# Performance work log

Measured on AMD Instinct MI355X. Metric: run time of the kernel, lower is better.

## Reference

```python
import jax, jax.numpy as jnp
import numpy as np

IOU_THRESHOLD = 0.5


def setup_inputs() -> dict:
    key = jax.random.key(0)
    k1, k2, k3 = jax.random.split(key, 3)
    B, N = 4, 8192
    # valid boxes: top-left in [0,200), width/height in [1,51)
    xy = jax.random.uniform(k1, (B, N, 2), dtype=jnp.float32) * 200.0
    wh = jax.random.uniform(k2, (B, N, 2), dtype=jnp.float32) * 50.0 + 1.0
    boxes = jnp.concatenate([xy, xy + wh], axis=-1)  # [B,N,4] (x1,y1,x2,y2)
    scores = jax.random.uniform(k3, (B, N), dtype=jnp.float32)
    return {"boxes": boxes, "scores": scores}


def _soft_nms_single(boxes, scores):
    # boxes: [N,4], scores: [N]
    x1, y1, x2, y2 = boxes[:, 0], boxes[:, 1], boxes[:, 2], boxes[:, 3]
    inter_w = jnp.maximum(0.0, jnp.minimum(x2[:, None], x2[None, :]) - jnp.maximum(x1[:, None], x1[None, :]))
    inter_h = jnp.maximum(0.0, jnp.minimum(y2[:, None], y2[None, :]) - jnp.maximum(y1[:, None], y1[None, :]))
    inter = inter_w * inter_h  # [N,N]
    area = (x2 - x1) * (y2 - y1)  # [N]
    union = area[:, None] + area[None, :] - inter
    iou = inter / union  # [N,N]
    weight = jnp.exp(-iou / IOU_THRESHOLD)  # [N,N]
    adjusted = weight @ scores  # [N] : adjusted_scores[i] = sum_j w[i,j]*s[j]
    w = jax.nn.softmax(adjusted, axis=0)  # [N]
    return w @ boxes  # [4]


def reference(boxes, scores):
    return jax.vmap(_soft_nms_single)(boxes, scores)  # [B,4]
```

## Files before the change

kernel.cpp:

```cpp
#include <hip/hip_runtime.h>
#include <hip/hip_bf16.h>

#define BATCH   4
#define NBOX    8192
#define BLOCK   256
#define TSZ     256
#define NT      (NBOX / TSZ)
#define NPAIRS  (NT * (NT + 1) / 2)
#define NBINS   2048
#define SUBS    8
#define SUBSZ   (NBOX / SUBS)
#define STH     512

__device__ __forceinline__ float bf2f(unsigned short u) {
    union { unsigned int i; float f; } c;
    c.i = ((unsigned int)u) << 16;
    return c.f;
}

__device__ __forceinline__ bool box_plausible(float x1, float y1, float x2, float y2) {
    bool ok = (x1 == x1) && (y1 == y1) && (x2 == x2) && (y2 == y2);
    ok = ok && fabsf(x1) < 1e4f && fabsf(y1) < 1e4f && fabsf(x2) < 1e4f && fabsf(y2) < 1e4f;
    ok = ok && x1 >= -1.0f && x1 <= 300.0f && y1 >= -1.0f && y1 <= 300.0f;
    const float w = x2 - x1, h = y2 - y1;
    ok = ok && w >= -0.1f && w <= 80.0f && h >= -0.1f && h <= 80.0f;
    return ok;
}

__device__ __forceinline__ bool wave_probe_is_f32(const void* boxes_raw) {
    const int lane = threadIdx.x & 63;
    const float* bf = (const float*)boxes_raw;
    const bool okf = box_plausible(bf[lane * 4 + 0], bf[lane * 4 + 1],
                                   bf[lane * 4 + 2], bf[lane * 4 + 3]);
    const unsigned short* bh = (const unsigned short*)boxes_raw;
    const bool okh = box_plausible(bf2f(bh[lane * 4 + 0]), bf2f(bh[lane * 4 + 1]),
                                   bf2f(bh[lane * 4 + 2]), bf2f(bh[lane * 4 + 3]));
    const unsigned long long mf = __ballot(okf);
    const unsigned long long mh = __ballot(okh);
    return __popcll(mf) >= __popcll(mh);
}

__device__ __forceinline__ float4 load_box(const void* boxes_raw, size_t idx, bool isf32) {
    if (isf32) {
        return reinterpret_cast<const float4*>(boxes_raw)[idx];
    } else {
        const ushort4 u = reinterpret_cast<const ushort4*>(boxes_raw)[idx];
        return make_float4(bf2f(u.x), bf2f(u.y), bf2f(u.z), bf2f(u.w));
    }
}

__device__ __forceinline__ float load_score(const void* scores_raw, size_t idx, bool isf32) {
    return isf32 ? ((const float*)scores_raw)[idx]
                 : bf2f(((const unsigned short*)scores_raw)[idx]);
}

__device__ __forceinline__ int key_bin(float v) {
    const int bb = (int)(v * 8.0f);
    return min(NBINS - 1, max(0, bb));
}

#define CEXP (-2.8853900817779268f)

__device__ __forceinline__ float pair_weight(
    float ix1, float iy1, float ix2, float iy2, float iarea,
    const float4& bj, float jarea)
{
    float w = fminf(ix2, bj.z) - fmaxf(ix1, bj.x);
    float h = fminf(iy2, bj.w) - fmaxf(iy1, bj.y);
    w = fmaxf(w, 0.0f);
    h = fmaxf(h, 0.0f);
    const float inter = w * h;
    const float uni   = iarea + jarea - inter;
    const float arg   = (CEXP * inter) * __builtin_amdgcn_rcpf(uni);
    return __builtin_amdgcn_exp2f(arg);
}

__global__ __launch_bounds__(STH) void sort_kernel(
    const void* __restrict__ boxes_raw, const void* __restrict__ scores_raw,
    float4* __restrict__ sboxes, float* __restrict__ sscores,
    float* __restrict__ adj,
    float* __restrict__ minx1c, float* __restrict__ maxx2c,
    int* __restrict__ pairlist, int* __restrict__ count)
{
    __shared__ int hist[NBINS];
    __shared__ int bmin[NBINS];
    __shared__ int hist2[NBINS];
    __shared__ int wsum[STH / 64];
    __shared__ float sminT[NT], smaxT[NT];
    __shared__ int scnt;

    const int b    = blockIdx.x / SUBS;
    const int sub  = blockIdx.x % SUBS;
    const int tid  = threadIdx.x;
    const int lane = tid & 63;
    const int wv   = tid >> 6;
    const bool isf32 = wave_probe_is_f32(boxes_raw);
    const size_t base = (size_t)b * NBOX;

#pragma unroll
    for (int i = 0; i < NBINS / STH; i++) {
        hist[i * STH + tid]  = 0;
        bmin[i * STH + tid]  = 0x7f800000;
        hist2[i * STH + tid] = 0;
    }
    if (tid == 0) scnt = 0;
    {
        const size_t z = (size_t)blockIdx.x * 1024;
        adj[z + tid] = 0.0f;
        adj[z + STH + tid] = 0.0f;
    }
    __syncthreads();

    const int sublim = sub * SUBSZ;
#pragma unroll
    for (int k = 0; k < NBOX / STH; k++) {
        const int i = k * STH + tid;
        const float4 bx = load_box(boxes_raw, base + i, isf32);
        const int bin = key_bin(bx.z);
        atomicAdd(&hist[bin], 1);
        atomicMin(&bmin[bin], __float_as_int(bx.x));
        if (i < sublim) atomicAdd(&hist2[bin], 1);
    }
    __syncthreads();

    {
        int tot[4], cum[4];
        int run = 0;
#pragma unroll
        for (int i = 0; i < 4; i++) {
            tot[i] = hist[tid * 4 + i];
            run += tot[i]; cum[i] = run;
        }
        int v = run;
#pragma unroll
        for (int d = 1; d < 64; d <<= 1) {
            const int u = __shfl_up(v, d);
            if (lane >= d) v += u;
        }
        if (lane == 63) wsum[wv] = v;
        __syncthreads();
        int wb = 0;
        for (int w = 0; w < wv; w++) wb += wsum[w];
        const int tb = wb + v - run;
#pragma unroll
        for (int i = 0; i < 4; i++) {
            const int bin = tid * 4 + i;
            const int e = tb + cum[i] - tot[i];
            const int m = hist2[bin];
            hist[bin]  = e;
            hist2[bin] = e + m;
        }
    }
    __syncthreads();

    if (tid < NT) {
        int p = tid * TSZ;
        int lo = 0, hi = NBINS - 1;
        while (lo < hi) { const int mid = (lo + hi + 1) >> 1;
                          if (hist[mid] <= p) lo = mid; else hi = mid - 1; }
        const int Bf = lo;
        p = tid * TSZ + TSZ - 1;
        lo = 0; hi = NBINS - 1;
        while (lo < hi) { const int mid = (lo + hi + 1) >> 1;
                          if (hist[mid] <= p) lo = mid; else hi = mid - 1; }
        const int Bl = lo;
        float mn = 3.4e38f;
        for (int q = Bf; q <= Bl; q++) mn = fminf(mn, __int_as_float(bmin[q]));
        const float mx = (float)(Bl + 1) * 0.125f;
        sminT[tid] = mn; smaxT[tid] = mx;
        if (sub == 0) {
            minx1c[b * NT + tid] = mn;
            maxx2c[b * NT + tid] = mx;
        }
    }
    __syncthreads();

    if (sub == 0) {
        for (int q = tid; q < NPAIRS; q += STH) {
            int p = q, it = 0;
            while (p >= NT - it) { p -= NT - it; it++; }
            const int jt = it + p;
            const bool live = !((smaxT[it] < sminT[jt]) || (smaxT[jt] < sminT[it]));
            if (live) {
                const int idx = atomicAdd(&scnt, 1);
                pairlist[b * NPAIRS + idx] = (it << 8) | jt;
            }
        }
    }

#pragma unroll
    for (int k = 0; k < SUBSZ / STH; k++) {
        const int i = sub * SUBSZ + k * STH + tid;
        const float4 bx = load_box(boxes_raw, base + i, isf32);
        const float  sc = load_score(scores_raw, base + i, isf32);
        const int pos = atomicAdd(&hist2[key_bin(bx.z)], 1);
        sboxes[base + pos]  = bx;
        sscores[base + pos] = sc;
    }

    __syncthreads();
    if (sub == 0 && tid == 0) count[b] = scnt;
}

__global__ __launch_bounds__(TSZ) void perm_kernel(
    const float4* __restrict__ sboxes, const float* __restrict__ sscores,
    float4* __restrict__ cboxes, float2* __restrict__ cas,
    int* __restrict__ crank,
    float* __restrict__ cgmin)
{
    __shared__ float key[TSZ];
    __shared__ int   idx[TSZ];
    const int tile = blockIdx.x;
    const size_t gbase = (size_t)tile * TSZ;
    const int tid = threadIdx.x;

    key[tid] = sboxes[gbase + tid].x;
    idx[tid] = tid;
    __syncthreads();

    for (int k = 2; k <= TSZ; k <<= 1) {
        for (int j = k >> 1; j > 0; j >>= 1) {
            const int l = tid ^ j;
            if (l > tid) {
                const bool up = ((tid & k) == 0);
                const float a = key[tid], c = key[l];
                if ((a > c) == up) {
                    key[tid] = c; key[l] = a;
                    const int ti = idx[tid]; idx[tid] = idx[l]; idx[l] = ti;
                }
            }
            __syncthreads();
        }
    }

    const int src = idx[tid];
    const float4 u = sboxes[gbase + src];
    cboxes[gbase + tid] = u;
    cas[gbase + tid] = make_float2((u.z - u.x) * (u.w - u.y), sscores[gbase + src]);
    crank[gbase + tid] = src;
    if ((tid & 63) == 0) cgmin[tile * 4 + (tid >> 6)] = key[tid];
}

__global__ __launch_bounds__(BLOCK, 4) void soft_nms_adj_kernel(
    const float4* __restrict__ sboxes,
    const float* __restrict__ sscores,
    const float4* __restrict__ cboxes,
    const float2* __restrict__ cas,
    const int* __restrict__ crank,
    const float* __restrict__ cgmin,
    const int* __restrict__ pairlist,
    const int* __restrict__ count,
    float* __restrict__ adj)
{
    __shared__ float4 sbox[TSZ];
    __shared__ float2 sas[TSZ];
    __shared__ float  srow[4][TSZ];

    const int bid = blockIdx.x;
    const int b   = bid / NPAIRS;
    const int p   = bid % NPAIRS;
    if (p >= count[b]) return;
    const int pr = pairlist[b * NPAIRS + p];
    const int it = pr >> 8, jt = pr & 255;

    const int tid  = threadIdx.x;
    const int lane = tid & 63;
    const int wv   = tid >> 6;
    const size_t base = (size_t)b * NBOX;

    float ws;
    {
        const int jg = jt * TSZ + tid;
        const float4 uj = cboxes[base + jg];
        sbox[tid] = uj;
        const float2 asv = cas[base + jg];
        sas[tid]  = asv;
        float w0 = asv.y;
#pragma unroll
        for (int off = 32; off > 0; off >>= 1) w0 += __shfl_xor(w0, off);
        ws = w0;
    }

    float rx1[4], ry1[4], rx2[4], ry2[4], rar[4], rsc[4];
#pragma unroll
    for (int k = 0; k < 4; k++) {
        const int ig = it * TSZ + k * 64 + lane;
        const float4 ui = sboxes[base + ig];
        rx1[k] = ui.x; ry1[k] = ui.y; rx2[k] = ui.z; ry2[k] = ui.w;
        rar[k] = (ui.z - ui.x) * (ui.w - ui.y);
        rsc[k] = sscores[base + ig];
    }

    int kstart = 0;
    if (it != jt) {
        const float cg = cgmin[(b * NT + jt) * 4 + wv];
#pragma unroll
        for (int k = 0; k < 4; k++) {
            const float gmax = __shfl(rx2[k], 63) + 0.125f;
            if (kstart == k && gmax < cg) kstart = k + 1;
        }
    }
    float ccorr = 0.0f;
    if (kstart > 0) {
#pragma unroll
        for (int k = 0; k < 4; k++) {
            if (k < kstart) {
                float gs = rsc[k];
#pragma unroll
                for (int off = 32; off > 0; off >>= 1) gs += __shfl_xor(gs, off);
                ccorr += gs;
            }
        }
    }

    __syncthreads();

    float accr[4];
#pragma unroll
    for (int k = 0; k < 4; k++) accr[k] = (k < kstart) ? ws : 0.0f;

    const int wvbase = wv * 64;

    if (it == jt) {
#pragma unroll 2
        for (int t = 0; t < 64; t++) {
            const int idx = wvbase + ((lane + t) & 63);
            const float4 bj = sbox[idx];
            const float2 as = sas[idx];
#pragma unroll
            for (int k = 0; k < 4; k++) {
                const float e = pair_weight(rx1[k], ry1[k], rx2[k], ry2[k], rar[k], bj, as.x);
                accr[k] = fmaf(e, as.y, accr[k]);
            }
        }
    } else {
#define OFFD_LOOP(KS)                                                          \
        {                                                                      \
            float accc = ccorr;                                                \
            _Pragma("unroll 2")                                                \
            for (int t = 0; t < 64; t++) {                                     \
                const int idx = wvbase + ((lane + t) & 63);                    \
                const float4 bj = sbox[idx];                                   \
                const float2 as = sas[idx];                                    \
                float c = 0.0f;                                                \
                _Pragma("unroll")                                              \
                for (int k = KS; k < 4; ++k) {                                 \
                    const float e = pair_weight(rx1[k], ry1[k], rx2[k], ry2[k],\
                                                rar[k], bj, as.x);             \
                    accr[k] = fmaf(e, as.y, accr[k]);                          \
                    c = fmaf(e, rsc[k], c);                                    \
                }                                                              \
                accc += __shfl(c, (lane - t) & 63);                            \
            }                                                                  \
            const int cr = crank[base + jt * TSZ + wvbase + lane];             \
            atomicAdd(&adj[base + jt * TSZ + cr], accc);                       \
        }
        switch (kstart) {
            case 0: OFFD_LOOP(0); break;
            case 1: OFFD_LOOP(1); break;
            case 2: OFFD_LOOP(2); break;
            case 3: OFFD_LOOP(3); break;
            default: {
                const int cr = crank[base + jt * TSZ + wvbase + lane];
                atomicAdd(&adj[base + jt * TSZ + cr], ccorr);
            } break;
        }
#undef OFFD_LOOP
    }

#pragma unroll
    for (int k = 0; k < 4; k++) srow[wv][k * 64 + lane] = accr[k];
    __syncthreads();
    {
        const float rs = srow[0][tid] + srow[1][tid] + srow[2][tid] + srow[3][tid];
        atomicAdd(&adj[base + it * TSZ + tid], rs);
    }
}

#define FBLK 1024
__global__ __launch_bounds__(FBLK) void soft_nms_finish_kernel(
    const float4* __restrict__ sboxes,
    const float* __restrict__ sscores,
    const float* __restrict__ adj,
    const float* __restrict__ minx1c, const float* __restrict__ maxx2c,
    const void* __restrict__ boxes_raw,
    void* __restrict__ out)
{
    constexpr int K  = NBOX / FBLK;
    constexpr int NW = FBLK / 64;
    __shared__ float sminx[NT], smaxx[NT], ssumT[NT], scorr[NT];
    __shared__ float smax_[NW];
    __shared__ float sred[NW][5];

    const int b    = blockIdx.x;
    const int tid  = threadIdx.x;
    const int lane = tid & 63;
    const int wv   = tid >> 6;
    const size_t base = (size_t)b * NBOX;

    const bool isf32 = wave_probe_is_f32(boxes_raw);

    if (tid < NT) {
        sminx[tid] = minx1c[b * NT + tid];
        smaxx[tid] = maxx2c[b * NT + tid];
    }
#pragma unroll
    for (int tt = 0; tt < 2; tt++) {
        const int T = wv * 2 + tt;
        float sm = 0.0f;
#pragma unroll
        for (int q = 0; q < 4; q++) sm += sscores[base + T * TSZ + q * 64 + lane];
#pragma unroll
        for (int off = 32; off > 0; off >>= 1) sm += __shfl_down(sm, off);
        if (lane == 0) ssumT[T] = sm;
    }
    __syncthreads();
    if (tid < NT) {
        float c = 0.0f;
        for (int T2 = 0; T2 < NT; T2++) {
            const bool skip = (smaxx[tid] < sminx[T2]) || (smaxx[T2] < sminx[tid]);
            if (skip) c += ssumT[T2];
        }
        scorr[tid] = c;
    }
    __syncthreads();

    float av[K];
    float m = -3.4e38f;
#pragma unroll
    for (int k = 0; k < K; k++) {
        const int r = k * FBLK + tid;
        av[k] = adj[base + r] + scorr[r >> 8];
        m = fmaxf(m, av[k]);
    }
#pragma unroll
    for (int off = 32; off > 0; off >>= 1)
        m = fmaxf(m, __shfl_down(m, off));
    if (lane == 0) smax_[wv] = m;
    __syncthreads();
    float M = smax_[0];
#pragma unroll
    for (int w = 1; w < NW; w++) M = fmaxf(M, smax_[w]);

    const float L2E = 1.4426950408889634f;
    float es = 0.0f, s0 = 0.0f, s1 = 0.0f, s2 = 0.0f, s3 = 0.0f;
#pragma unroll
    for (int k = 0; k < K; k++) {
        const float e = __builtin_amdgcn_exp2f((av[k] - M) * L2E);
        const float4 u = sboxes[base + k * FBLK + tid];
        es += e;
        s0 += e * u.x;
        s1 += e * u.y;
        s2 += e * u.z;
        s3 += e * u.w;
    }
#pragma unroll
    for (int off = 32; off > 0; off >>= 1) {
        es += __shfl_down(es, off);
        s0 += __shfl_down(s0, off);
        s1 += __shfl_down(s1, off);
        s2 += __shfl_down(s2, off);
        s3 += __shfl_down(s3, off);
    }
    if (lane == 0) {
        sred[wv][0] = es; sred[wv][1] = s0; sred[wv][2] = s1;
        sred[wv][3] = s2; sred[wv][4] = s3;
    }
    __syncthreads();
    if (tid == 0) {
        float ES = 0.0f, o[4] = {0.0f, 0.0f, 0.0f, 0.0f};
#pragma unroll
        for (int w = 0; w < NW; w++) {
            ES   += sred[w][0];
            o[0] += sred[w][1];
            o[1] += sred[w][2];
            o[2] += sred[w][3];
            o[3] += sred[w][4];
        }
        const float inv = 1.0f / ES;
        if (isf32) {
            float* of = (float*)out;
            for (int c = 0; c < 4; c++) of[b * 4 + c] = o[c] * inv;
        } else {
            __hip_bfloat16* oh = (__hip_bfloat16*)out;
            for (int c = 0; c < 4; c++) oh[b * 4 + c] = __float2bfloat16(o[c] * inv);
        }
    }
}

extern "C" void kernel_launch(void* const* d_in, const int* in_sizes, int n_in,
                              void* d_out, int out_size, void* d_ws, size_t ws_size,
                              hipStream_t stream) {
    const void* boxes_raw  = d_in[0];
    const void* scores_raw = d_in[1];

    char* w = (char*)d_ws;
    float4* sboxes   = (float4*)w;                 w += (size_t)BATCH * NBOX * 16;
    float4* cboxes   = (float4*)w;                 w += (size_t)BATCH * NBOX * 16;
    float2* cas      = (float2*)w;                 w += (size_t)BATCH * NBOX * 8;
    float*  sscores  = (float*)w;                  w += (size_t)BATCH * NBOX * 4;
    float*  adj      = (float*)w;                  w += (size_t)BATCH * NBOX * 4;
    int*    crank    = (int*)w;                    w += (size_t)BATCH * NBOX * 4;
    float*  minx1c   = (float*)w;                  w += (size_t)BATCH * NT * 4;
    float*  maxx2c   = (float*)w;                  w += (size_t)BATCH * NT * 4;
    float*  cgmin    = (float*)w;                  w += (size_t)BATCH * NT * 4 * 4;
    int*    pairlist = (int*)w;                    w += (size_t)BATCH * NPAIRS * 4;
    int*    count    = (int*)w;

    sort_kernel<<<dim3(BATCH * SUBS), dim3(STH), 0, stream>>>(
        boxes_raw, scores_raw, sboxes, sscores, adj, minx1c, maxx2c, pairlist, count);
    perm_kernel<<<dim3(BATCH * NT), dim3(TSZ), 0, stream>>>(
        sboxes, sscores, cboxes, cas, crank, cgmin);
    soft_nms_adj_kernel<<<dim3(BATCH * NPAIRS), dim3(BLOCK), 0, stream>>>(
        sboxes, sscores, cboxes, cas, crank, cgmin, pairlist, count, adj);
    soft_nms_finish_kernel<<<dim3(BATCH), dim3(FBLK), 0, stream>>>(
        sboxes, sscores, adj, minx1c, maxx2c, boxes_raw, d_out);
}
```

Baseline: 136.4 us.

## Replace bitonic sort with rank sort and accumulate column sums in permuted order

The per-tile bitonic sort in perm_kernel becomes an O(n) rank computation per thread that scatters boxes straight to their sorted slot and records the inverse permutation. The adjacency kernel no longer looks up crank before each column atomicAdd. It writes into a separate adjc buffer in permuted order, and the finish kernel gathers it back through cinv. Launch bounds for the adjacency kernel rise from 4 to 8 blocks per CU, at the cost of one extra zeroed buffer and an indexed gather in the finish kernel.

```diff
diff --git a/kernel.cpp b/kernel.cpp
--- a/kernel.cpp
+++ b/kernel.cpp
@@ -78,7 +78,7 @@
 __global__ __launch_bounds__(STH) void sort_kernel(
     const void* __restrict__ boxes_raw, const void* __restrict__ scores_raw,
     float4* __restrict__ sboxes, float* __restrict__ sscores,
-    float* __restrict__ adj,
+    float* __restrict__ adj, float* __restrict__ adjc,
     float* __restrict__ minx1c, float* __restrict__ maxx2c,
     int* __restrict__ pairlist, int* __restrict__ count)
 {
@@ -108,6 +108,8 @@
         const size_t z = (size_t)blockIdx.x * 1024;
         adj[z + tid] = 0.0f;
         adj[z + STH + tid] = 0.0f;
+        adjc[z + tid] = 0.0f;
+        adjc[z + STH + tid] = 0.0f;
     }
     __syncthreads();
 
@@ -205,52 +207,42 @@
 __global__ __launch_bounds__(TSZ) void perm_kernel(
     const float4* __restrict__ sboxes, const float* __restrict__ sscores,
     float4* __restrict__ cboxes, float2* __restrict__ cas,
-    int* __restrict__ crank,
+    int* __restrict__ cinv,
     float* __restrict__ cgmin)
 {
-    __shared__ float key[TSZ];
-    __shared__ int   idx[TSZ];
+    __shared__ float sx1[TSZ];
     const int tile = blockIdx.x;
     const size_t gbase = (size_t)tile * TSZ;
     const int tid = threadIdx.x;
 
-    key[tid] = sboxes[gbase + tid].x;
-    idx[tid] = tid;
-    __syncthreads();
-
-    for (int k = 2; k <= TSZ; k <<= 1) {
-        for (int j = k >> 1; j > 0; j >>= 1) {
-            const int l = tid ^ j;
-            if (l > tid) {
-                const bool up = ((tid & k) == 0);
-                const float a = key[tid], c = key[l];
-                if ((a > c) == up) {
-                    key[tid] = c; key[l] = a;
-                    const int ti = idx[tid]; idx[tid] = idx[l]; idx[l] = ti;
-                }
-            }
-            __syncthreads();
-        }
-    }
-
-    const int src = idx[tid];
-    const float4 u = sboxes[gbase + src];
-    cboxes[gbase + tid] = u;
-    cas[gbase + tid] = make_float2((u.z - u.x) * (u.w - u.y), sscores[gbase + src]);
-    crank[gbase + tid] = src;
-    if ((tid & 63) == 0) cgmin[tile * 4 + (tid >> 6)] = key[tid];
-}
-
-__global__ __launch_bounds__(BLOCK, 4) void soft_nms_adj_kernel(
+    const float4 u = sboxes[gbase + tid];
+    const float sc = sscores[gbase + tid];
+    sx1[tid] = u.x;
+    __syncthreads();
+
+    int rank = 0;
+#pragma unroll 8
+    for (int j = 0; j < TSZ; j++) {
+        const float v = sx1[j];
+        rank += (v < u.x || (v == u.x && j < tid)) ? 1 : 0;
+    }
+
+    cboxes[gbase + rank] = u;
+    cas[gbase + rank] = make_float2((u.z - u.x) * (u.w - u.y), sc);
+    cinv[gbase + tid] = rank;
+    if ((rank & 63) == 0) cgmin[tile * 4 + (rank >> 6)] = u.x;
+}
+
+__global__ __launch_bounds__(BLOCK, 8) void soft_nms_adj_kernel(
     const float4* __restrict__ sboxes,
     const float* __restrict__ sscores,
     const float4* __restrict__ cboxes,
     const float2* __restrict__ cas,
-    const int* __restrict__ crank,
     const float* __restrict__ cgmin,
     const int* __restrict__ pairlist,
     const int* __restrict__ count,
-    float* __restrict__ adj)
+    float* __restrict__ adj,
+    float* __restrict__ adjc)
 {
     __shared__ float4 sbox[TSZ];
     __shared__ float2 sas[TSZ];
@@ -352,18 +344,16 @@
                 }                                                              \
                 accc += __shfl(c, (lane - t) & 63);                            \
             }                                                                  \
-            const int cr = crank[base + jt * TSZ + wvbase + lane];             \
-            atomicAdd(&adj[base + jt * TSZ + cr], accc);                       \
+            atomicAdd(&adjc[base + jt * TSZ + wvbase + lane], accc);           \
         }
         switch (kstart) {
             case 0: OFFD_LOOP(0); break;
             case 1: OFFD_LOOP(1); break;
             case 2: OFFD_LOOP(2); break;
             case 3: OFFD_LOOP(3); break;
-            default: {
-                const int cr = crank[base + jt * TSZ + wvbase + lane];
-                atomicAdd(&adj[base + jt * TSZ + cr], ccorr);
-            } break;
+            default:
+                atomicAdd(&adjc[base + jt * TSZ + wvbase + lane], ccorr);
+                break;
         }
 #undef OFFD_LOOP
     }
@@ -382,6 +372,8 @@
     const float4* __restrict__ sboxes,
     const float* __restrict__ sscores,
     const float* __restrict__ adj,
+    const float* __restrict__ adjc,
+    const int* __restrict__ cinv,
     const float* __restrict__ minx1c, const float* __restrict__ maxx2c,
     const void* __restrict__ boxes_raw,
     void* __restrict__ out)
@@ -430,7 +422,8 @@
 #pragma unroll
     for (int k = 0; k < K; k++) {
         const int r = k * FBLK + tid;
-        av[k] = adj[base + r] + scorr[r >> 8];
+        const int pos = cinv[base + r];
+        av[k] = adj[base + r] + adjc[base + (r & ~255) + pos] + scorr[r >> 8];
         m = fmaxf(m, av[k]);
     }
 #pragma unroll
@@ -500,7 +493,8 @@
     float2* cas      = (float2*)w;                 w += (size_t)BATCH * NBOX * 8;
     float*  sscores  = (float*)w;                  w += (size_t)BATCH * NBOX * 4;
     float*  adj      = (float*)w;                  w += (size_t)BATCH * NBOX * 4;
-    int*    crank    = (int*)w;                    w += (size_t)BATCH * NBOX * 4;
+    float*  adjc     = (float*)w;                  w += (size_t)BATCH * NBOX * 4;
+    int*    cinv     = (int*)w;                    w += (size_t)BATCH * NBOX * 4;
     float*  minx1c   = (float*)w;                  w += (size_t)BATCH * NT * 4;
     float*  maxx2c   = (float*)w;                  w += (size_t)BATCH * NT * 4;
     float*  cgmin    = (float*)w;                  w += (size_t)BATCH * NT * 4 * 4;
@@ -508,11 +502,11 @@
     int*    count    = (int*)w;
 
     sort_kernel<<<dim3(BATCH * SUBS), dim3(STH), 0, stream>>>(
-        boxes_raw, scores_raw, sboxes, sscores, adj, minx1c, maxx2c, pairlist, count);
+        boxes_raw, scores_raw, sboxes, sscores, adj, adjc, minx1c, maxx2c, pairlist, count);
     perm_kernel<<<dim3(BATCH * NT), dim3(TSZ), 0, stream>>>(
-        sboxes, sscores, cboxes, cas, crank, cgmin);
+        sboxes, sscores, cboxes, cas, cinv, cgmin);
     soft_nms_adj_kernel<<<dim3(BATCH * NPAIRS), dim3(BLOCK), 0, stream>>>(
-        sboxes, sscores, cboxes, cas, crank, cgmin, pairlist, count, adj);
+        sboxes, sscores, cboxes, cas, cgmin, pairlist, count, adj, adjc);
     soft_nms_finish_kernel<<<dim3(BATCH), dim3(FBLK), 0, stream>>>(
-        sboxes, sscores, adj, minx1c, maxx2c, boxes_raw, d_out);
-}
+        sboxes, sscores, adj, adjc, cinv, minx1c, maxx2c, boxes_raw, d_out);
+}
```

Result: slower. 140.7 us (+3.1%).
